# Optimization experiments

Hardware: AMD Instinct MI355X
Metric: run time of the kernel (lower is better)

## Reference

```python
import jax, jax.numpy as jnp
import numpy as np

N = 100000
E = 1_600_000
EPS = 1e-5
NEG_SLOPE = 0.01


def leaky_relu(x):
    return jnp.where(x > 0, x, NEG_SLOPE * x)


def batchnorm(x, gamma, beta):
    # BatchNorm1d in training mode: batch statistics, biased variance
    m = jnp.mean(x, axis=0)
    v = jnp.mean((x - m) ** 2, axis=0)
    return (x - m) * jax.lax.rsqrt(v + EPS) * gamma + beta


def gcn_conv(x, W, b, src, dst, norm, n):
    # PyG GCNConv: h = x @ W; aggregate norm * h[src] into dst; add bias
    h = x @ W                              # [N, F_out]
    msgs = h[src] * norm[:, None]          # [E', F_out] gather + scale
    out = jax.ops.segment_sum(msgs, dst, num_segments=n)  # scatter-add
    return out + b


def setup_inputs() -> dict:
    key = jax.random.key(0)
    ks = jax.random.split(key, 14)
    d_in, d_h1, d_h2, d_out = 128, 128, 64, 8
    x = jax.random.normal(ks[0], (N, d_in), dtype=jnp.float32)
    edge_index = jax.random.randint(ks[1], (2, E), 0, N, dtype=jnp.int64)
    edge_weights = jax.random.uniform(ks[2], (E,), dtype=jnp.float32)
    # Glorot-ish init for GCNConv weights, zero bias (PyG default bias=True)
    W1 = jax.random.normal(ks[3], (d_in, d_h1), dtype=jnp.float32) / np.sqrt(d_in)
    b1 = jnp.zeros((d_h1,), jnp.float32)
    W2 = jax.random.normal(ks[4], (d_h1, d_h2), dtype=jnp.float32) / np.sqrt(d_h1)
    b2 = jnp.zeros((d_h2,), jnp.float32)
    W3 = jax.random.normal(ks[5], (d_h2, d_out), dtype=jnp.float32) / np.sqrt(d_h2)
    b3 = jnp.zeros((d_out,), jnp.float32)
    gamma1 = jnp.ones((d_h1,), jnp.float32)
    beta1 = jnp.zeros((d_h1,), jnp.float32)
    gamma2 = jnp.ones((d_h2,), jnp.float32)
    beta2 = jnp.zeros((d_h2,), jnp.float32)
    return {"x": x, "edge_index": edge_index, "edge_weights": edge_weights,
            "W1": W1, "b1": b1, "W2": W2, "b2": b2, "W3": W3, "b3": b3,
            "gamma1": gamma1, "beta1": beta1, "gamma2": gamma2, "beta2": beta2}


def reference(x, edge_index, edge_weights, W1, b1, W2, b2, W3, b3,
              gamma1, beta1, gamma2, beta2):
    # edge_weights is accepted (as in the original forward signature) but unused:
    # the module calls GCNConv(x, edge_index) without weights.
    n = x.shape[0]
    loop = jnp.arange(n, dtype=edge_index.dtype)
    src = jnp.concatenate([edge_index[0], loop])  # add self-loops
    dst = jnp.concatenate([edge_index[1], loop])
    # symmetric normalization with unit edge weights (in-degree on dst)
    deg = jax.ops.segment_sum(jnp.ones_like(dst, dtype=x.dtype), dst,
                              num_segments=n)
    dinv = jnp.where(deg > 0, jax.lax.rsqrt(deg), 0.0)
    norm = dinv[src] * dinv[dst]

    h = leaky_relu(gcn_conv(x, W1, b1, src, dst, norm, n))
    h = batchnorm(h, gamma1, beta1)
    h = leaky_relu(gcn_conv(h, W2, b2, src, dst, norm, n))
    h = batchnorm(h, gamma2, beta2)
    h = leaky_relu(gcn_conv(h, W3, b3, src, dst, norm, n))
    return h
```

## Files before the change

### kernel.cpp

```cpp
#include <hip/hip_runtime.h>
#include <cstdint>
#include <cstddef>

#define NEG_SLOPE 0.01f
#define BN_EPS 1e-5f
#define BSHIFT 6
#define BMASK 63
#define NBLK 128

using short8 = __attribute__((ext_vector_type(8))) short;
using f32x4 = __attribute__((ext_vector_type(4))) float;

__device__ inline unsigned short f2bf(float f) {
    unsigned int u = __float_as_uint(f);
    u += 0x7FFFu + ((u >> 16) & 1u);
    return (unsigned short)(u >> 16);
}


__global__ __launch_bounds__(1024) void pre_kernel(const int* __restrict__ dst,
                                                   int* __restrict__ hist,
                                                   int E, int nb, int chunk,
                                                   const float* __restrict__ W1,
                                                   unsigned short* __restrict__ wt1,
                                                   const float* __restrict__ W2,
                                                   unsigned short* __restrict__ wt2) {
    const int b = blockIdx.x;
    if (b < NBLK) {
        __shared__ int lh[2048];
        for (int i = threadIdx.x; i < nb; i += 1024) lh[i] = 0;
        __syncthreads();
        const int e0 = b * chunk;
        const int e1 = min(E, e0 + chunk);
        for (int e = e0 + threadIdx.x; e < e1; e += 1024)
            atomicAdd(&lh[dst[e] >> BSHIFT], 1);
        __syncthreads();
        for (int k = threadIdx.x; k < nb; k += 1024)
            hist[k * NBLK + b] = lh[k];
    } else {
        int idx = (b - NBLK) * 1024 + threadIdx.x;
        if (idx < 128 * 128) {
            int k = idx >> 7, n = idx & 127;
            wt1[n * 128 + k] = f2bf(W1[idx]);
        } else if (idx < 128 * 128 + 128 * 64) {
            int j = idx - 128 * 128;
            int k = j >> 6, n = j & 63;
            wt2[n * 128 + k] = f2bf(W2[j]);
        }
    }
}

__global__ __launch_bounds__(1024) void scan_block_kernel(const int* __restrict__ in,
                                                          int* __restrict__ out,
                                                          int* __restrict__ partials, int n) {
    __shared__ int sm[1024];
    int tid = threadIdx.x;
    int i = blockIdx.x * 1024 + tid;
    int v = (i < n) ? in[i] : 0;
    int x = v;
    sm[tid] = x;
    __syncthreads();
    for (int off = 1; off < 1024; off <<= 1) {
        int y = (tid >= off) ? sm[tid - off] : 0;
        __syncthreads();
        x += y;
        sm[tid] = x;
        __syncthreads();
    }
    if (i < n) out[i] = x - v;
    if (tid == 1023) partials[blockIdx.x] = x;
}

__global__ __launch_bounds__(1024) void chunkscatter_kernel(const int* __restrict__ src,
                                                            const int* __restrict__ dst,
                                                            const int* __restrict__ S,
                                                            const int* __restrict__ partials,
                                                            unsigned int* __restrict__ packed,
                                                            int E, int nb, int chunk, int MB) {
    __shared__ int cur[2048];
    __shared__ int pof[256];
    const int b = blockIdx.x;
    if (threadIdx.x == 0) {
        int acc = 0;
        for (int i = 0; i < MB; ++i) { pof[i] = acc; acc += partials[i]; }
    }
    __syncthreads();
    for (int k = threadIdx.x; k < nb; k += 1024) {
        const int i = k * NBLK + b;
        cur[k] = S[i] + pof[i >> 10];
    }
    __syncthreads();
    const int e0 = b * chunk;
    const int e1 = min(E, e0 + chunk);
    for (int e = e0 + threadIdx.x; e < e1; e += 1024) {
        int d = dst[e];
        int slot = atomicAdd(&cur[d >> BSHIFT], 1);
        packed[slot] = ((unsigned int)src[e] << BSHIFT) | (unsigned int)(d & BMASK);
    }
}

__global__ __launch_bounds__(256) void bucket_build_kernel(const unsigned int* __restrict__ packed,
                                                           const int* __restrict__ S,
                                                           const int* __restrict__ partials,
                                                           int* __restrict__ rowptr,
                                                           float* __restrict__ dinv,
                                                           int* __restrict__ csr,
                                                           int N, int nb, int E, int MB) {
    const int b = blockIdx.x;
    const int t = threadIdx.x;
    __shared__ int pof[256];
    __shared__ int eb[2];
    if (t == 0) {
        int acc = 0;
        for (int i = 0; i < MB; ++i) { pof[i] = acc; acc += partials[i]; }
        const int i0 = b * NBLK;
        eb[0] = S[i0] + pof[i0 >> 10];
        if (b == nb - 1) eb[1] = E;
        else {
            const int i1 = (b + 1) * NBLK;
            eb[1] = S[i1] + pof[i1 >> 10];
        }
    }
    __syncthreads();
    const int e0 = eb[0], e1 = eb[1];
    const int node0 = b << BSHIFT;
    __shared__ int hist[64], cur[64];
    if (t < 64) hist[t] = 0;
    __syncthreads();
    for (int e = e0 + t; e < e1; e += 256)
        atomicAdd(&hist[packed[e] & BMASK], 1);
    __syncthreads();
    if (t < 64) {
        int h = hist[t];
        int v = h;
        for (int o = 1; o < 64; o <<= 1) {
            int y = __shfl_up(v, o);
            if (t >= o) v += y;
        }
        int base = e0 + v - h;
        int node = node0 + t;
        if (node < N) {
            rowptr[node] = base;
            dinv[node] = rsqrtf((float)(h + 1));
        }
        cur[t] = base;
    }
    if (b == nb - 1 && t == 0) rowptr[N] = E;
    __syncthreads();
    for (int e = e0 + t; e < e1; e += 256) {
        unsigned int p = packed[e];
        int slot = atomicAdd(&cur[p & BMASK], 1);
        csr[slot] = (int)(p >> BSHIFT);
    }
}


template <int MF, bool BN, bool XBF>
__global__ __launch_bounds__(256) void mgemm_kernel(const void* __restrict__ Xv,
                                                    const unsigned short* __restrict__ Wt,
                                                    const float* __restrict__ bnS,
                                                    const float* __restrict__ bnT,
                                                    const float* __restrict__ dinv,
                                                    unsigned short* __restrict__ H, int n) {
    constexpr int K = 128;
    constexpr int CTW = (MF / 16) / 4;
    __shared__ unsigned short Xl[64 * K];
    __shared__ unsigned short Wl[MF * K];
    __shared__ float dl[64];

    const int t = threadIdx.x;
    const int wave = t >> 6;
    const int lane = t & 63;
    const int row0 = blockIdx.x * 64;

    if (XBF) {
        const unsigned short* X = (const unsigned short*)Xv;
        for (int idx = t; idx < 64 * K / 8; idx += 256) {
            int r = idx >> 4, c8 = idx & 15;
            int row = row0 + r; if (row >= n) row = n - 1;
            uint4 v = ((const uint4*)(X + (size_t)row * K))[c8];
            float xv[8];
            xv[0] = __uint_as_float(v.x << 16); xv[1] = __uint_as_float(v.x & 0xFFFF0000u);
            xv[2] = __uint_as_float(v.y << 16); xv[3] = __uint_as_float(v.y & 0xFFFF0000u);
            xv[4] = __uint_as_float(v.z << 16); xv[5] = __uint_as_float(v.z & 0xFFFF0000u);
            xv[6] = __uint_as_float(v.w << 16); xv[7] = __uint_as_float(v.w & 0xFFFF0000u);
            if (BN) {
                const float4 s0 = ((const float4*)bnS)[c8 * 2];
                const float4 s1 = ((const float4*)bnS)[c8 * 2 + 1];
                const float4 t0 = ((const float4*)bnT)[c8 * 2];
                const float4 t1 = ((const float4*)bnT)[c8 * 2 + 1];
                xv[0] = xv[0] * s0.x + t0.x; xv[1] = xv[1] * s0.y + t0.y;
                xv[2] = xv[2] * s0.z + t0.z; xv[3] = xv[3] * s0.w + t0.w;
                xv[4] = xv[4] * s1.x + t1.x; xv[5] = xv[5] * s1.y + t1.y;
                xv[6] = xv[6] * s1.z + t1.z; xv[7] = xv[7] * s1.w + t1.w;
            }
            uint4 o;
            o.x = (unsigned)f2bf(xv[0]) | ((unsigned)f2bf(xv[1]) << 16);
            o.y = (unsigned)f2bf(xv[2]) | ((unsigned)f2bf(xv[3]) << 16);
            o.z = (unsigned)f2bf(xv[4]) | ((unsigned)f2bf(xv[5]) << 16);
            o.w = (unsigned)f2bf(xv[6]) | ((unsigned)f2bf(xv[7]) << 16);
            *(uint4*)((char*)Xl + r * 256 + ((c8 * 16) ^ ((r & 7) << 4))) = o;
        }
    } else {
        const float* X = (const float*)Xv;
        for (int idx = t; idx < 64 * K / 4; idx += 256) {
            int r = idx >> 5, c4 = idx & 31;
            int row = row0 + r; if (row >= n) row = n - 1;
            float4 v = ((const float4*)(X + (size_t)row * K))[c4];
            if (BN) {
                float4 sv = ((const float4*)bnS)[c4];
                float4 tv = ((const float4*)bnT)[c4];
                v.x = v.x * sv.x + tv.x; v.y = v.y * sv.y + tv.y;
                v.z = v.z * sv.z + tv.z; v.w = v.w * sv.w + tv.w;
            }
            ushort4 o; o.x = f2bf(v.x); o.y = f2bf(v.y); o.z = f2bf(v.z); o.w = f2bf(v.w);
            *(ushort4*)((char*)Xl + r * 256 + ((c4 * 8) ^ ((r & 7) << 4))) = o;
        }
    }
    for (int idx = t; idx < MF * K / 4; idx += 256) {
        int nr = idx >> 5, k4 = idx & 31;
        ushort4 o = ((const ushort4*)(Wt + (size_t)nr * K))[k4];
        *(ushort4*)((char*)Wl + nr * 256 + ((k4 * 8) ^ ((nr & 7) << 4))) = o;
    }
    if (t < 64) { int row = row0 + t; dl[t] = dinv[row < n ? row : n - 1]; }
    __syncthreads();

    f32x4 acc[CTW][4];
#pragma unroll
    for (int c = 0; c < CTW; ++c)
#pragma unroll
        for (int rt = 0; rt < 4; ++rt)
            acc[c][rt] = (f32x4){0.f, 0.f, 0.f, 0.f};

    const int kg = lane >> 4;
    const int lr = lane & 15;

#pragma unroll
    for (int kk = 0; kk < 4; ++kk) {
        const int kb = (kk * 32 + kg * 8) * 2;
        short8 a[4];
#pragma unroll
        for (int rt = 0; rt < 4; ++rt) {
            int r = rt * 16 + lr;
            a[rt] = *(const short8*)((const char*)Xl + r * 256 + (kb ^ ((r & 7) << 4)));
        }
#pragma unroll
        for (int c = 0; c < CTW; ++c) {
            int nr = (wave * CTW + c) * 16 + lr;
            short8 b = *(const short8*)((const char*)Wl + nr * 256 + (kb ^ ((nr & 7) << 4)));
#pragma unroll
            for (int rt = 0; rt < 4; ++rt)
                acc[c][rt] = __builtin_amdgcn_mfma_f32_16x16x32_bf16(a[rt], b, acc[c][rt], 0, 0, 0);
        }
    }
    __syncthreads();

    unsigned short* Ol = (unsigned short*)Xl;
#pragma unroll
    for (int c = 0; c < CTW; ++c) {
        int col = (wave * CTW + c) * 16 + lr;
#pragma unroll
        for (int rt = 0; rt < 4; ++rt) {
#pragma unroll
            for (int j = 0; j < 4; ++j) {
                int r = rt * 16 + kg * 4 + j;
                Ol[r * MF + col] = f2bf(acc[c][rt][j] * dl[r]);
            }
        }
    }
    __syncthreads();
    for (int idx = t; idx < 64 * MF / 4; idx += 256) {
        int r = idx / (MF / 4), c4 = idx % (MF / 4);
        int row = row0 + r;
        if (row < n)
            ((ushort4*)(H + (size_t)row * MF))[c4] = ((const ushort4*)Ol)[idx];
    }
}


__global__ __launch_bounds__(256) void gemm3_kernel(const unsigned short* __restrict__ X,
                                                    const float* __restrict__ W,
                                                    const float* __restrict__ bnS,
                                                    const float* __restrict__ bnT,
                                                    const float* __restrict__ dinv,
                                                    unsigned short* __restrict__ H, int n) {
    __shared__ float Wl[512];
    __shared__ float sl[64], tl[64];
    const int t = threadIdx.x;
    for (int i = t; i < 512; i += 256) Wl[i] = W[i];
    if (t < 64) { sl[t] = bnS[t]; tl[t] = bnT[t]; }
    __syncthreads();
    const int node = blockIdx.x * 256 + t;
    if (node >= n) return;
    float acc[8];
#pragma unroll
    for (int m = 0; m < 8; ++m) acc[m] = 0.f;
    const uint4* xp = (const uint4*)(X + (size_t)node * 64);
#pragma unroll
    for (int c8 = 0; c8 < 8; ++c8) {
        const uint4 v = xp[c8];
        float xv[8];
        xv[0] = __uint_as_float(v.x << 16); xv[1] = __uint_as_float(v.x & 0xFFFF0000u);
        xv[2] = __uint_as_float(v.y << 16); xv[3] = __uint_as_float(v.y & 0xFFFF0000u);
        xv[4] = __uint_as_float(v.z << 16); xv[5] = __uint_as_float(v.z & 0xFFFF0000u);
        xv[6] = __uint_as_float(v.w << 16); xv[7] = __uint_as_float(v.w & 0xFFFF0000u);
#pragma unroll
        for (int j = 0; j < 8; ++j) {
            const int k = c8 * 8 + j;
            const float x = xv[j] * sl[k] + tl[k];
#pragma unroll
            for (int m = 0; m < 8; ++m) acc[m] += x * Wl[k * 8 + m];
        }
    }
    const float di = dinv[node];
    uint4 o;
    o.x = (unsigned)f2bf(acc[0] * di) | ((unsigned)f2bf(acc[1] * di) << 16);
    o.y = (unsigned)f2bf(acc[2] * di) | ((unsigned)f2bf(acc[3] * di) << 16);
    o.z = (unsigned)f2bf(acc[4] * di) | ((unsigned)f2bf(acc[5] * di) << 16);
    o.w = (unsigned)f2bf(acc[6] * di) | ((unsigned)f2bf(acc[7] * di) << 16);
    *(uint4*)(H + (size_t)node * 8) = o;
}


template <int F, int GROUP, bool BF16OUT>
__global__ __launch_bounds__(256) void agg_kernel(const unsigned short* __restrict__ h,
                                                  const int* __restrict__ rowptr,
                                                  const int* __restrict__ csr,
                                                  const float* __restrict__ dinv,
                                                  const float* __restrict__ bias,
                                                  void* __restrict__ yout, int n) {
    constexpr int NPB = 256 / GROUP;
    const int g = threadIdx.x % GROUP;
    const int node = blockIdx.x * NPB + threadIdx.x / GROUP;
    if (node >= n) return;
    const int f0 = g * 8;
    const unsigned short* hp = h + f0;
    float a0 = 0.f, a1 = 0.f, a2 = 0.f, a3 = 0.f, a4 = 0.f, a5 = 0.f, a6 = 0.f, a7 = 0.f;
#define ACC8(v)                                    \
    a0 += __uint_as_float((v).x << 16);            \
    a1 += __uint_as_float((v).x & 0xFFFF0000u);    \
    a2 += __uint_as_float((v).y << 16);            \
    a3 += __uint_as_float((v).y & 0xFFFF0000u);    \
    a4 += __uint_as_float((v).z << 16);            \
    a5 += __uint_as_float((v).z & 0xFFFF0000u);    \
    a6 += __uint_as_float((v).w << 16);            \
    a7 += __uint_as_float((v).w & 0xFFFF0000u);
    int e = rowptr[node];
    const int r1 = rowptr[node + 1];
    for (; e + 4 <= r1; e += 4) {
        const int s0 = csr[e], s1 = csr[e + 1], s2 = csr[e + 2], s3 = csr[e + 3];
        const uint4 v0 = *(const uint4*)(hp + (size_t)s0 * F);
        const uint4 v1 = *(const uint4*)(hp + (size_t)s1 * F);
        const uint4 v2 = *(const uint4*)(hp + (size_t)s2 * F);
        const uint4 v3 = *(const uint4*)(hp + (size_t)s3 * F);
        ACC8(v0); ACC8(v1); ACC8(v2); ACC8(v3);
    }
    for (; e < r1; ++e) {
        const int s = csr[e];
        const uint4 v = *(const uint4*)(hp + (size_t)s * F);
        ACC8(v);
    }
    {
        const uint4 v = *(const uint4*)(hp + (size_t)node * F);
        ACC8(v);
    }
#undef ACC8
    const float di = dinv[node];
    const float4 bA = *(const float4*)(bias + f0);
    const float4 bB = *(const float4*)(bias + f0 + 4);
    float r[8];
    r[0] = di * a0 + bA.x; r[1] = di * a1 + bA.y;
    r[2] = di * a2 + bA.z; r[3] = di * a3 + bA.w;
    r[4] = di * a4 + bB.x; r[5] = di * a5 + bB.y;
    r[6] = di * a6 + bB.z; r[7] = di * a7 + bB.w;
#pragma unroll
    for (int k = 0; k < 8; ++k) r[k] = r[k] > 0.f ? r[k] : NEG_SLOPE * r[k];
    if (BF16OUT) {
        uint4 o;
        o.x = (unsigned)f2bf(r[0]) | ((unsigned)f2bf(r[1]) << 16);
        o.y = (unsigned)f2bf(r[2]) | ((unsigned)f2bf(r[3]) << 16);
        o.z = (unsigned)f2bf(r[4]) | ((unsigned)f2bf(r[5]) << 16);
        o.w = (unsigned)f2bf(r[6]) | ((unsigned)f2bf(r[7]) << 16);
        *(uint4*)((unsigned short*)yout + (size_t)node * F + f0) = o;
    } else {
        float4 o0, o1;
        o0.x = r[0]; o0.y = r[1]; o0.z = r[2]; o0.w = r[3];
        o1.x = r[4]; o1.y = r[5]; o1.z = r[6]; o1.w = r[7];
        float* yp = (float*)yout + (size_t)node * F + f0;
        *(float4*)(yp) = o0;
        *(float4*)(yp + 4) = o1;
    }
}


template <int F>
__global__ __launch_bounds__(256) void bstats_kernel(const unsigned short* __restrict__ y,
                                                     float* __restrict__ sumP,
                                                     float* __restrict__ ssqP,
                                                     int n, int nblocks) {
    constexpr int GROUP = F / 8;
    constexpr int NPB = 256 / GROUP;
    const int g = threadIdx.x % GROUP;
    const int slot = threadIdx.x / GROUP;
    const int f0 = g * 8;
    float ss[8], qq[8];
#pragma unroll
    for (int k = 0; k < 8; ++k) { ss[k] = 0.f; qq[k] = 0.f; }
    for (int base = blockIdx.x * NPB; base < n; base += nblocks * NPB) {
        const int node = base + slot;
        if (node < n) {
            const uint4 v = *(const uint4*)(y + (size_t)node * F + f0);
            float xv[8];
            xv[0] = __uint_as_float(v.x << 16); xv[1] = __uint_as_float(v.x & 0xFFFF0000u);
            xv[2] = __uint_as_float(v.y << 16); xv[3] = __uint_as_float(v.y & 0xFFFF0000u);
            xv[4] = __uint_as_float(v.z << 16); xv[5] = __uint_as_float(v.z & 0xFFFF0000u);
            xv[6] = __uint_as_float(v.w << 16); xv[7] = __uint_as_float(v.w & 0xFFFF0000u);
#pragma unroll
            for (int k = 0; k < 8; ++k) { ss[k] += xv[k]; qq[k] += xv[k] * xv[k]; }
        }
    }
    __shared__ float smS[F], smQ[F];
    for (int i = threadIdx.x; i < F; i += 256) { smS[i] = 0.f; smQ[i] = 0.f; }
    __syncthreads();
#pragma unroll
    for (int k = 0; k < 8; ++k) {
        atomicAdd(&smS[f0 + k], ss[k]);
        atomicAdd(&smQ[f0 + k], qq[k]);
    }
    __syncthreads();
    for (int i = threadIdx.x; i < F; i += 256) {
        sumP[(size_t)blockIdx.x * F + i] = smS[i];
        ssqP[(size_t)blockIdx.x * F + i] = smQ[i];
    }
}


__global__ __launch_bounds__(256) void bnparam_kernel(const float* __restrict__ sumP,
                                                      const float* __restrict__ ssqP,
                                                      const float* __restrict__ gamma,
                                                      const float* __restrict__ beta,
                                                      float* __restrict__ S, float* __restrict__ T,
                                                      int n, int F, int NB) {
    const int f = blockIdx.x;
    const int t = threadIdx.x;
    float s = 0.f, q = 0.f;
    for (int b = t; b < NB; b += 256) {
        s += sumP[(size_t)b * F + f];
        q += ssqP[(size_t)b * F + f];
    }
    __shared__ float rs[4], rq[4];
    for (int o = 32; o; o >>= 1) { s += __shfl_down(s, o); q += __shfl_down(q, o); }
    if ((t & 63) == 0) { rs[t >> 6] = s; rq[t >> 6] = q; }
    __syncthreads();
    if (t == 0) {
        s = rs[0] + rs[1] + rs[2] + rs[3];
        q = rq[0] + rq[1] + rq[2] + rq[3];
        const float m = s / (float)n;
        const float var = q / (float)n - m * m;
        const float inv = rsqrtf(var + BN_EPS);
        const float sc = gamma[f] * inv;
        S[f] = sc;
        T[f] = beta[f] - m * sc;
    }
}


extern "C" void kernel_launch(void* const* d_in, const int* in_sizes, int n_in,
                              void* d_out, int out_size, void* d_ws, size_t ws_size,
                              hipStream_t stream) {
    const float* x = (const float*)d_in[0];
    const int* edges = (const int*)d_in[1];
    const float* W1 = (const float*)d_in[3];
    const float* b1 = (const float*)d_in[4];
    const float* W2 = (const float*)d_in[5];
    const float* b2 = (const float*)d_in[6];
    const float* W3 = (const float*)d_in[7];
    const float* b3 = (const float*)d_in[8];
    const float* gamma1 = (const float*)d_in[9];
    const float* beta1 = (const float*)d_in[10];
    const float* gamma2 = (const float*)d_in[11];
    const float* beta2 = (const float*)d_in[12];

    const int N = in_sizes[0] / 128;
    const int E = in_sizes[1] / 2;
    const int* esrc = edges;
    const int* edst = edges + E;
    const int nb = (N + BMASK) >> BSHIFT;
    const int M = nb * NBLK;
    const int chunk = (E + NBLK - 1) / NBLK;
    const int NBS = 1024;

    char* ws = (char*)d_ws;
    size_t off = 0;
    auto alloc = [&](size_t bytes) -> void* {
        void* p = ws + off;
        off = (off + bytes + 255) & ~(size_t)255;
        return p;
    };
    int* hist = (int*)alloc((size_t)M * 4);
    int* S = (int*)alloc((size_t)M * 4);
    int* partials = (int*)alloc(1024 * 4);
    int* rowptr = (int*)alloc((size_t)(N + 1) * 4);
    float* dinv = (float*)alloc((size_t)N * 4);
    float* bn = (float*)alloc(512 * 4);
    float* sumP1 = (float*)alloc((size_t)NBS * 128 * 4);
    float* ssqP1 = (float*)alloc((size_t)NBS * 128 * 4);
    float* sumP2 = (float*)alloc((size_t)NBS * 64 * 4);
    float* ssqP2 = (float*)alloc((size_t)NBS * 64 * 4);
    unsigned short* wt1 = (unsigned short*)alloc(128 * 128 * 2);
    unsigned short* wt2 = (unsigned short*)alloc(64 * 128 * 2);
    int* csr = (int*)alloc((size_t)E * 4);
    unsigned short* hbuf = (unsigned short*)alloc((size_t)N * 128 * 2);
    unsigned short* ybuf = (unsigned short*)alloc((size_t)N * 128 * 2);
    unsigned int* packed = (unsigned int*)hbuf;

    float* sA = bn;
    float* tA = bn + 128;
    float* sB = bn + 256;
    float* tB = bn + 384;

    const int MB = (M + 1023) / 1024;
    const int TBLK = (128 * 128 + 128 * 64 + 1023) / 1024;

    pre_kernel<<<NBLK + TBLK, 1024, 0, stream>>>(edst, hist, E, nb, chunk, W1, wt1, W2, wt2);
    scan_block_kernel<<<MB, 1024, 0, stream>>>(hist, S, partials, M);
    chunkscatter_kernel<<<NBLK, 1024, 0, stream>>>(esrc, edst, S, partials, packed, E, nb, chunk, MB);
    bucket_build_kernel<<<nb, 256, 0, stream>>>(packed, S, partials, rowptr, dinv, csr, N, nb, E, MB);

    mgemm_kernel<128, false, false><<<(N + 63) / 64, 256, 0, stream>>>(x, wt1, nullptr, nullptr, dinv, hbuf, N);
    agg_kernel<128, 16, true><<<(N + 15) / 16, 256, 0, stream>>>(hbuf, rowptr, csr, dinv, b1, ybuf, N);
    bstats_kernel<128><<<NBS, 256, 0, stream>>>(ybuf, sumP1, ssqP1, N, NBS);
    bnparam_kernel<<<128, 256, 0, stream>>>(sumP1, ssqP1, gamma1, beta1, sA, tA, N, 128, NBS);

    mgemm_kernel<64, true, true><<<(N + 63) / 64, 256, 0, stream>>>(ybuf, wt2, sA, tA, dinv, hbuf, N);
    agg_kernel<64, 8, true><<<(N + 31) / 32, 256, 0, stream>>>(hbuf, rowptr, csr, dinv, b2, ybuf, N);
    bstats_kernel<64><<<NBS, 256, 0, stream>>>(ybuf, sumP2, ssqP2, N, NBS);
    bnparam_kernel<<<64, 256, 0, stream>>>(sumP2, ssqP2, gamma2, beta2, sB, tB, N, 64, NBS);

    gemm3_kernel<<<(N + 255) / 256, 256, 0, stream>>>(ybuf, W3, sB, tB, dinv, hbuf, N);
    agg_kernel<8, 1, false><<<(N + 255) / 256, 256, 0, stream>>>(hbuf, rowptr, csr, dinv, b3, (float*)d_out, N);
}
```

Baseline: 268.9 us.

## Fuse BN parameter reduction into stats kernel and sort CSR neighbors by source bucket

Removes the separate bnparam kernel launches by having the last-finishing bstats block (detected with a global atomic counter plus threadfence) reduce the per-block partials and write the BN scale and shift. Separately, the bucket build now counts edges by (local dst, source range of 8192 nodes), so within each row the CSR neighbors are roughly grouped by source index. The aim is more local gathers in the aggregation kernels. The trade-off is a serial 1024-iteration reduction in one block and a heavier shared-memory histogram with a block-wide scan.

```diff
diff --git a/kernel.cpp b/kernel.cpp
--- a/kernel.cpp
+++ b/kernel.cpp
@@ -24,8 +24,10 @@
                                                    const float* __restrict__ W1,
                                                    unsigned short* __restrict__ wt1,
                                                    const float* __restrict__ W2,
-                                                   unsigned short* __restrict__ wt2) {
+                                                   unsigned short* __restrict__ wt2,
+                                                   int* __restrict__ ctr) {
     const int b = blockIdx.x;
+    if (b == 0 && threadIdx.x < 2) ctr[threadIdx.x] = 0;
     if (b < NBLK) {
         __shared__ int lh[2048];
         for (int i = threadIdx.x; i < nb; i += 1024) lh[i] = 0;
@@ -124,33 +126,55 @@
     __syncthreads();
     const int e0 = eb[0], e1 = eb[1];
     const int node0 = b << BSHIFT;
-    __shared__ int hist[64], cur[64];
-    if (t < 64) hist[t] = 0;
-    __syncthreads();
-    for (int e = e0 + t; e < e1; e += 256)
-        atomicAdd(&hist[packed[e] & BMASK], 1);
+    __shared__ int h2[1024];
+    __shared__ int tsum[256];
+    for (int i = t; i < 1024; i += 256) h2[i] = 0;
+    __syncthreads();
+    for (int e = e0 + t; e < e1; e += 256) {
+        const unsigned int p = packed[e];
+        const int ldst = p & BMASK;
+        int s4 = (int)(p >> BSHIFT) >> 13;
+        if (s4 > 15) s4 = 15;
+        atomicAdd(&h2[(ldst << 4) | s4], 1);
+    }
+    __syncthreads();
+    const int v0 = h2[4 * t], v1 = h2[4 * t + 1], v2 = h2[4 * t + 2], v3 = h2[4 * t + 3];
+    const int tot = v0 + v1 + v2 + v3;
+    int x = tot;
+    tsum[t] = x;
+    __syncthreads();
+    for (int o = 1; o < 256; o <<= 1) {
+        int y = (t >= o) ? tsum[t - o] : 0;
+        __syncthreads();
+        x += y;
+        tsum[t] = x;
+        __syncthreads();
+    }
+    const int base = e0 + x - tot;
+    h2[4 * t] = base;
+    h2[4 * t + 1] = base + v0;
+    h2[4 * t + 2] = base + v0 + v1;
+    h2[4 * t + 3] = base + v0 + v1 + v2;
     __syncthreads();
     if (t < 64) {
-        int h = hist[t];
-        int v = h;
-        for (int o = 1; o < 64; o <<= 1) {
-            int y = __shfl_up(v, o);
-            if (t >= o) v += y;
-        }
-        int base = e0 + v - h;
-        int node = node0 + t;
+        const int gs = h2[t << 4];
+        const int ge = (t == 63) ? e1 : h2[(t + 1) << 4];
+        const int node = node0 + t;
         if (node < N) {
-            rowptr[node] = base;
-            dinv[node] = rsqrtf((float)(h + 1));
-        }
-        cur[t] = base;
+            rowptr[node] = gs;
+            dinv[node] = rsqrtf((float)(ge - gs + 1));
+        }
     }
     if (b == nb - 1 && t == 0) rowptr[N] = E;
     __syncthreads();
     for (int e = e0 + t; e < e1; e += 256) {
-        unsigned int p = packed[e];
-        int slot = atomicAdd(&cur[p & BMASK], 1);
-        csr[slot] = (int)(p >> BSHIFT);
+        const unsigned int p = packed[e];
+        const int ldst = p & BMASK;
+        const int src = (int)(p >> BSHIFT);
+        int s4 = src >> 13;
+        if (s4 > 15) s4 = 15;
+        const int slot = atomicAdd(&h2[(ldst << 4) | s4], 1);
+        csr[slot] = src;
     }
 }
 
@@ -397,6 +421,11 @@
 __global__ __launch_bounds__(256) void bstats_kernel(const unsigned short* __restrict__ y,
                                                      float* __restrict__ sumP,
                                                      float* __restrict__ ssqP,
+                                                     const float* __restrict__ gamma,
+                                                     const float* __restrict__ beta,
+                                                     float* __restrict__ Sv,
+                                                     float* __restrict__ Tv,
+                                                     int* __restrict__ ctr,
                                                      int n, int nblocks) {
     constexpr int GROUP = F / 8;
     constexpr int NPB = 256 / GROUP;
@@ -432,35 +461,30 @@
         sumP[(size_t)blockIdx.x * F + i] = smS[i];
         ssqP[(size_t)blockIdx.x * F + i] = smQ[i];
     }
-}
-
-
-__global__ __launch_bounds__(256) void bnparam_kernel(const float* __restrict__ sumP,
-                                                      const float* __restrict__ ssqP,
-                                                      const float* __restrict__ gamma,
-                                                      const float* __restrict__ beta,
-                                                      float* __restrict__ S, float* __restrict__ T,
-                                                      int n, int F, int NB) {
-    const int f = blockIdx.x;
-    const int t = threadIdx.x;
-    float s = 0.f, q = 0.f;
-    for (int b = t; b < NB; b += 256) {
-        s += sumP[(size_t)b * F + f];
-        q += ssqP[(size_t)b * F + f];
-    }
-    __shared__ float rs[4], rq[4];
-    for (int o = 32; o; o >>= 1) { s += __shfl_down(s, o); q += __shfl_down(q, o); }
-    if ((t & 63) == 0) { rs[t >> 6] = s; rq[t >> 6] = q; }
-    __syncthreads();
-    if (t == 0) {
-        s = rs[0] + rs[1] + rs[2] + rs[3];
-        q = rq[0] + rq[1] + rq[2] + rq[3];
-        const float m = s / (float)n;
-        const float var = q / (float)n - m * m;
-        const float inv = rsqrtf(var + BN_EPS);
-        const float sc = gamma[f] * inv;
-        S[f] = sc;
-        T[f] = beta[f] - m * sc;
+    __threadfence();
+    __shared__ int isLast;
+    if (threadIdx.x == 0) {
+        const int old = atomicAdd(ctr, 1);
+        isLast = (old == nblocks - 1) ? 1 : 0;
+        if (isLast) *ctr = 0;
+    }
+    __syncthreads();
+    if (isLast) {
+        __threadfence();
+        const int f = threadIdx.x;
+        if (f < F) {
+            float s = 0.f, q = 0.f;
+            for (int bb = 0; bb < nblocks; ++bb) {
+                s += sumP[(size_t)bb * F + f];
+                q += ssqP[(size_t)bb * F + f];
+            }
+            const float m = s / (float)n;
+            const float var = q / (float)n - m * m;
+            const float inv = rsqrtf(var + BN_EPS);
+            const float sc = gamma[f] * inv;
+            Sv[f] = sc;
+            Tv[f] = beta[f] - m * sc;
+        }
     }
 }
 
@@ -500,6 +524,7 @@
     int* hist = (int*)alloc((size_t)M * 4);
     int* S = (int*)alloc((size_t)M * 4);
     int* partials = (int*)alloc(1024 * 4);
+    int* ctr = (int*)alloc(2 * 4);
     int* rowptr = (int*)alloc((size_t)(N + 1) * 4);
     float* dinv = (float*)alloc((size_t)N * 4);
     float* bn = (float*)alloc(512 * 4);
@@ -522,20 +547,18 @@
     const int MB = (M + 1023) / 1024;
     const int TBLK = (128 * 128 + 128 * 64 + 1023) / 1024;
 
-    pre_kernel<<<NBLK + TBLK, 1024, 0, stream>>>(edst, hist, E, nb, chunk, W1, wt1, W2, wt2);
+    pre_kernel<<<NBLK + TBLK, 1024, 0, stream>>>(edst, hist, E, nb, chunk, W1, wt1, W2, wt2, ctr);
     scan_block_kernel<<<MB, 1024, 0, stream>>>(hist, S, partials, M);
     chunkscatter_kernel<<<NBLK, 1024, 0, stream>>>(esrc, edst, S, partials, packed, E, nb, chunk, MB);
     bucket_build_kernel<<<nb, 256, 0, stream>>>(packed, S, partials, rowptr, dinv, csr, N, nb, E, MB);
 
     mgemm_kernel<128, false, false><<<(N + 63) / 64, 256, 0, stream>>>(x, wt1, nullptr, nullptr, dinv, hbuf, N);
     agg_kernel<128, 16, true><<<(N + 15) / 16, 256, 0, stream>>>(hbuf, rowptr, csr, dinv, b1, ybuf, N);
-    bstats_kernel<128><<<NBS, 256, 0, stream>>>(ybuf, sumP1, ssqP1, N, NBS);
-    bnparam_kernel<<<128, 256, 0, stream>>>(sumP1, ssqP1, gamma1, beta1, sA, tA, N, 128, NBS);
+    bstats_kernel<128><<<NBS, 256, 0, stream>>>(ybuf, sumP1, ssqP1, gamma1, beta1, sA, tA, ctr, N, NBS);
 
     mgemm_kernel<64, true, true><<<(N + 63) / 64, 256, 0, stream>>>(ybuf, wt2, sA, tA, dinv, hbuf, N);
     agg_kernel<64, 8, true><<<(N + 31) / 32, 256, 0, stream>>>(hbuf, rowptr, csr, dinv, b2, ybuf, N);
-    bstats_kernel<64><<<NBS, 256, 0, stream>>>(ybuf, sumP2, ssqP2, N, NBS);
-    bnparam_kernel<<<64, 256, 0, stream>>>(sumP2, ssqP2, gamma2, beta2, sB, tB, N, 64, NBS);
+    bstats_kernel<64><<<NBS, 256, 0, stream>>>(ybuf, sumP2, ssqP2, gamma2, beta2, sB, tB, ctr + 1, N, NBS);
 
     gemm3_kernel<<<(N + 255) / 256, 256, 0, stream>>>(ybuf, W3, sB, tB, dinv, hbuf, N);
     agg_kernel<8, 1, false><<<(N + 255) / 256, 256, 0, stream>>>(hbuf, rowptr, csr, dinv, b3, (float*)d_out, N);
```

New measurement: 841.5 us. 213% more time.
